# Performance work log

Hardware: AMD Instinct MI355X
Metric: run time of the kernel (lower is better)

The kernel has to match this reference:

```python
import jax, jax.numpy as jnp
import numpy as np

C, H, W = 128, 512, 512
YA, XA = 10, 10  # anchor grid; padded stats tables are (YA+2, XA+2)


def setup_inputs() -> dict:
    key = jax.random.key(0)
    k1, k2, k3 = jax.random.split(key, 3)
    x = jax.random.normal(k1, (2, C, H, W), jnp.float32)
    padded_mean_table = jax.random.normal(k2, (C, YA + 2, XA + 2), jnp.float32)
    # std table must be positive; keep away from zero
    padded_std_table = jax.random.uniform(k3, (C, YA + 2, XA + 2), jnp.float32) + 0.5
    weight = jnp.ones((1, C, 1, 1), jnp.float32)
    bias = jnp.zeros((1, C, 1, 1), jnp.float32)
    return {
        "x": x,
        "padded_mean_table": padded_mean_table,
        "padded_std_table": padded_std_table,
        "weight": weight,
        "bias": bias,
        "y_anchor": 3,
        "x_anchor": 4,
        "pre_y_anchor": 3,
        "pre_x_anchor": 5,
    }


def _axis_weights(n):
    # anchors of the 3x3 table sit at the centers of 3 tiles of size n;
    # we sample the pixels of the central tile. pos in (0.5, 1.5) in
    # anchor-index space -> bilinear between anchors (0,1) or (1,2).
    pos = (jnp.arange(n, dtype=jnp.float32) + 0.5) / n + 0.5
    i0 = jnp.floor(pos).astype(jnp.int32)  # 0 or 1
    w = pos - i0.astype(jnp.float32)
    return i0, w


def _interp3x3(table, h, w):
    # table: [C,3,3] -> [C,h,w] separable bilinear interpolation
    iy, wy = _axis_weights(h)
    ix, wx = _axis_weights(w)
    rows = table[:, iy, :] * (1.0 - wy)[None, :, None] + table[:, iy + 1, :] * wy[None, :, None]  # [C,h,3]
    out = rows[:, :, ix] * (1.0 - wx)[None, None, :] + rows[:, :, ix + 1] * wx[None, None, :]      # [C,h,w]
    return out


def reference(x, padded_mean_table, padded_std_table, weight, bias,
              y_anchor, x_anchor, pre_y_anchor, pre_x_anchor):
    real_x, pre_x = x[:1], x[1:]
    h, w = real_x.shape[2], real_x.shape[3]

    # --- pre_x branch: compute stats, scatter into padded tables, normalize ---
    pre_mean = jnp.mean(pre_x, axis=(2, 3))           # [1,C]
    pre_std = jnp.std(pre_x, axis=(2, 3), ddof=1)      # torch.std_mean default: unbiased
    pmt = padded_mean_table.at[:, pre_y_anchor + 1, pre_x_anchor + 1].set(pre_mean[0])
    pst = padded_std_table.at[:, pre_y_anchor + 1, pre_x_anchor + 1].set(pre_std[0])
    pre_out = (pre_x - pre_mean[:, :, None, None]) / pre_std[:, :, None, None] * weight + bias

    # --- real_x branch: gather 3x3 stats window, mask zeros with center, interpolate ---
    m = pmt[:, y_anchor:y_anchor + 3, x_anchor:x_anchor + 3]   # [C,3,3]
    s = pst[:, y_anchor:y_anchor + 3, x_anchor:x_anchor + 3]   # [C,3,3]
    m = jnp.where(m == 0, m[:, 1:2, 1:2], m)
    s = jnp.where(s == 0, s[:, 1:2, 1:2], s)
    m_map = _interp3x3(m, h, w)[None]          # [1,C,H,W]
    s_inv_map = _interp3x3(1.0 / s, h, w)[None]  # inverse-std interpolation
    real_out = (real_x - m_map) * s_inv_map * weight + bias

    return jnp.concatenate([real_out, pre_out], axis=0)
```

## Files before the change

### kernel.cpp

```cpp
#include <hip/hip_runtime.h>

constexpr int Cc  = 128;
constexpr int Hh  = 512;
constexpr int Ww  = 512;
constexpr int HW  = Hh * Ww;
constexpr int CHW = Cc * HW;
constexpr int NCHUNK = 16;

typedef float f32x4 __attribute__((ext_vector_type(4)));

__global__ __launch_bounds__(256) void pdin_reduce(const float* __restrict__ x,
                                                   float* __restrict__ partials) {
    const int c = blockIdx.y, chunk = blockIdx.x, tid = threadIdx.x;
    const f32x4* src = reinterpret_cast<const f32x4*>(
        x + (size_t)CHW + (size_t)c * HW + (size_t)chunk * 16384);
    float s = 0.f, q = 0.f;
#pragma unroll
    for (int i = 0; i < 16; ++i) {
        f32x4 v = src[tid + i * 256];
        s += (v.x + v.y) + (v.z + v.w);
        q += (v.x * v.x + v.y * v.y) + (v.z * v.z + v.w * v.w);
    }
#pragma unroll
    for (int off = 32; off; off >>= 1) {
        s += __shfl_down(s, off);
        q += __shfl_down(q, off);
    }
    __shared__ float ls[4], lq[4];
    const int wave = tid >> 6, lane = tid & 63;
    if (lane == 0) { ls[wave] = s; lq[wave] = q; }
    __syncthreads();
    if (tid == 0) {
        float S = (ls[0] + ls[1]) + (ls[2] + ls[3]);
        float Q = (lq[0] + lq[1]) + (lq[2] + lq[3]);
        partials[(c * NCHUNK + chunk) * 2 + 0] = S;
        partials[(c * NCHUNK + chunk) * 2 + 1] = Q;
    }
}

__global__ __launch_bounds__(256) void pdin_apply(const float* __restrict__ x,
                                                  const float* __restrict__ partials,
                                                  const float* __restrict__ mt,
                                                  const float* __restrict__ st,
                                                  const float* __restrict__ wgt,
                                                  const float* __restrict__ bia,
                                                  const int* __restrict__ ya_p,
                                                  const int* __restrict__ xa_p,
                                                  const int* __restrict__ pya_p,
                                                  const int* __restrict__ pxa_p,
                                                  float* __restrict__ out) {
    const int rblk = blockIdx.x;
    const int c    = blockIdx.y;
    const int half = blockIdx.z;

    float S = 0.f, Q = 0.f;
#pragma unroll
    for (int k = 0; k < NCHUNK; ++k) {
        S += partials[(c * NCHUNK + k) * 2 + 0];
        Q += partials[(c * NCHUNK + k) * 2 + 1];
    }
    const float Nf = (float)HW;
    const float mean = S / Nf;
    float var = (Q - S * mean) / (Nf - 1.0f);
    var = fmaxf(var, 0.0f);
    const float stdv = sqrtf(var);
    const float w = wgt[c], b = bia[c];

    const size_t cslab = (size_t)c * HW;
    const int base = rblk * 2048 + threadIdx.x;

    if (half == 0) {
        const float scale = w / stdv;
        const float shift = b - mean * scale;
        const f32x4* src = reinterpret_cast<const f32x4*>(x + (size_t)CHW + cslab);
        f32x4*       dst = reinterpret_cast<f32x4*>(out + (size_t)CHW + cslab);
        f32x4 v[8];
#pragma unroll
        for (int i = 0; i < 8; ++i) v[i] = src[base + i * 256];
#pragma unroll
        for (int i = 0; i < 8; ++i) {
            f32x4 o;
            o.x = v[i].x * scale + shift;
            o.y = v[i].y * scale + shift;
            o.z = v[i].z * scale + shift;
            o.w = v[i].w * scale + shift;
            __builtin_nontemporal_store(o, dst + base + i * 256);
        }
        return;
    }

    const int ya = ya_p[0], xa = xa_p[0];
    const int wr = pya_p[0] + 1, wc = pxa_p[0] + 1;
    const float* mtc = mt + c * 144;
    const float* stc = st + c * 144;

    const bool cw = (ya + 1 == wr) && (xa + 1 == wc);
    const float cm = cw ? mean : mtc[(ya + 1) * 12 + (xa + 1)];
    const float cs = cw ? stdv : stc[(ya + 1) * 12 + (xa + 1)];

    float G[9], R9[9];
#pragma unroll
    for (int r = 0; r < 3; ++r)
#pragma unroll
        for (int k = 0; k < 3; ++k) {
            const int Rr = ya + r, L = xa + k;
            const bool hit = (Rr == wr) && (L == wc);
            float mv = hit ? mean : mtc[Rr * 12 + L];
            if (mv == 0.0f) mv = cm;
            float sv = hit ? stdv : stc[Rr * 12 + L];
            if (sv == 0.0f) sv = cs;
            G[r * 3 + k]  = mv;
            R9[r * 3 + k] = 1.0f / sv;
        }

    const f32x4* src = reinterpret_cast<const f32x4*>(x + cslab);
    f32x4*       dst = reinterpret_cast<f32x4*>(out + cslab);
    constexpr float inv = 1.0f / 512.0f;

    f32x4 v[8];
#pragma unroll
    for (int i = 0; i < 8; ++i)
        v[i] = __builtin_nontemporal_load(src + base + i * 256);

#pragma unroll
    for (int i = 0; i < 8; ++i) {
        const int p  = base + i * 256;
        const int y  = p >> 7;
        const int xq = p & 127;
        const int iy = (y  >= 256) ? 1 : 0;
        const int ix = (xq >= 64)  ? 1 : 0;
        const float wy  = ((float)y + 0.5f) * inv + 0.5f - (float)iy;
        const float wx0 = ((float)(xq * 4) + 0.5f) * inv + 0.5f - (float)ix;

        const float a0 = iy ? G[3] : G[0], a1 = iy ? G[4] : G[1], a2 = iy ? G[5] : G[2];
        const float b0 = iy ? G[6] : G[3], b1 = iy ? G[7] : G[4], b2 = iy ? G[8] : G[5];
        const float mtL = ix ? a1 : a0, mtR = ix ? a2 : a1;
        const float mbL = ix ? b1 : b0, mbR = ix ? b2 : b1;
        const float u0 = iy ? R9[3] : R9[0], u1 = iy ? R9[4] : R9[1], u2 = iy ? R9[5] : R9[2];
        const float v0 = iy ? R9[6] : R9[3], v1 = iy ? R9[7] : R9[4], v2 = iy ? R9[8] : R9[5];
        const float stL = ix ? u1 : u0, stR = ix ? u2 : u1;
        const float sbL = ix ? v1 : v0, sbR = ix ? v2 : v1;

        const float omwy = 1.0f - wy;
        const float mrowL = mtL * omwy + mbL * wy;
        const float mrowR = mtR * omwy + mbR * wy;
        const float srowL = stL * omwy + sbL * wy;
        const float srowR = stR * omwy + sbR * wy;

        float r[4];
        const float in4[4] = { v[i].x, v[i].y, v[i].z, v[i].w };
#pragma unroll
        for (int j = 0; j < 4; ++j) {
            const float wx   = wx0 + (float)j * inv;
            const float omwx = 1.0f - wx;
            const float m_v  = mrowL * omwx + mrowR * wx;
            const float s_v  = srowL * omwx + srowR * wx;
            r[j] = (in4[j] - m_v) * s_v * w + b;
        }
        f32x4 o; o.x = r[0]; o.y = r[1]; o.z = r[2]; o.w = r[3];
        __builtin_nontemporal_store(o, dst + p);
    }
}

extern "C" void kernel_launch(void* const* d_in, const int* in_sizes, int n_in,
                              void* d_out, int out_size, void* d_ws, size_t ws_size,
                              hipStream_t stream) {
    const float* x   = (const float*)d_in[0];
    const float* mt  = (const float*)d_in[1];
    const float* st  = (const float*)d_in[2];
    const float* wgt = (const float*)d_in[3];
    const float* bia = (const float*)d_in[4];
    const int* ya  = (const int*)d_in[5];
    const int* xa  = (const int*)d_in[6];
    const int* pya = (const int*)d_in[7];
    const int* pxa = (const int*)d_in[8];
    float* out = (float*)d_out;

    float* partials = (float*)d_ws;

    pdin_reduce<<<dim3(NCHUNK, Cc), 256, 0, stream>>>(x, partials);
    pdin_apply<<<dim3(Hh / 16, Cc, 2), 256, 0, stream>>>(
        x, partials, mt, st, wgt, bia, ya, xa, pya, pxa, out);
}
```

Before: 109.3 us.

## Fuse reduce and apply into one persistent cooperative kernel with grid sync

Merges the statistics reduction and the normalization/interpolation pass into a single cooperative kernel. Persistent blocks loop over reduction chunks, meet at a grid-wide barrier, then loop over apply units. This removes the second kernel launch and the gap between the two kernels. In exchange it adds grid-sync overhead, host-side occupancy queries on every launch, and a grid capped at 2048 blocks, which may reduce memory-level parallelism.

```diff
diff --git a/kernel.cpp b/kernel.cpp
--- a/kernel.cpp
+++ b/kernel.cpp
@@ -1,4 +1,7 @@
 #include <hip/hip_runtime.h>
+#include <hip/hip_cooperative_groups.h>
+
+namespace cg = cooperative_groups;
 
 constexpr int Cc  = 128;
 constexpr int Hh  = 512;
@@ -6,159 +9,169 @@
 constexpr int HW  = Hh * Ww;
 constexpr int CHW = Cc * HW;
 constexpr int NCHUNK = 16;
+constexpr int NCHUNKS_TOTAL = Cc * NCHUNK;
+constexpr int NUNITS = 2 * Cc * 32;
 
 typedef float f32x4 __attribute__((ext_vector_type(4)));
 
-__global__ __launch_bounds__(256) void pdin_reduce(const float* __restrict__ x,
-                                                   float* __restrict__ partials) {
-    const int c = blockIdx.y, chunk = blockIdx.x, tid = threadIdx.x;
-    const f32x4* src = reinterpret_cast<const f32x4*>(
-        x + (size_t)CHW + (size_t)c * HW + (size_t)chunk * 16384);
-    float s = 0.f, q = 0.f;
-#pragma unroll
-    for (int i = 0; i < 16; ++i) {
-        f32x4 v = src[tid + i * 256];
-        s += (v.x + v.y) + (v.z + v.w);
-        q += (v.x * v.x + v.y * v.y) + (v.z * v.z + v.w * v.w);
+__global__ __launch_bounds__(256, 4) void pdin_fused(
+    const float* __restrict__ x,
+    float* __restrict__ partials,
+    const float* __restrict__ mt,
+    const float* __restrict__ st,
+    const float* __restrict__ wgt,
+    const float* __restrict__ bia,
+    const int* __restrict__ ya_p,
+    const int* __restrict__ xa_p,
+    const int* __restrict__ pya_p,
+    const int* __restrict__ pxa_p,
+    float* __restrict__ out)
+{
+    const int tid = threadIdx.x;
+    const int G   = gridDim.x;
+    __shared__ float ls[4], lq[4];
+
+    for (int cidx = blockIdx.x; cidx < NCHUNKS_TOTAL; cidx += G) {
+        const int c = cidx >> 4, chunk = cidx & 15;
+        const f32x4* src = reinterpret_cast<const f32x4*>(
+            x + (size_t)CHW + (size_t)c * HW + (size_t)chunk * 16384);
+        float s = 0.f, q = 0.f;
+#pragma unroll
+        for (int i = 0; i < 16; ++i) {
+            f32x4 v = src[tid + i * 256];
+            s += (v.x + v.y) + (v.z + v.w);
+            q += (v.x * v.x + v.y * v.y) + (v.z * v.z + v.w * v.w);
+        }
+#pragma unroll
+        for (int off = 32; off; off >>= 1) {
+            s += __shfl_down(s, off);
+            q += __shfl_down(q, off);
+        }
+        const int wave = tid >> 6, lane = tid & 63;
+        if (lane == 0) { ls[wave] = s; lq[wave] = q; }
+        __syncthreads();
+        if (tid == 0) {
+            partials[cidx * 2 + 0] = (ls[0] + ls[1]) + (ls[2] + ls[3]);
+            partials[cidx * 2 + 1] = (lq[0] + lq[1]) + (lq[2] + lq[3]);
+        }
+        __syncthreads();
     }
-#pragma unroll
-    for (int off = 32; off; off >>= 1) {
-        s += __shfl_down(s, off);
-        q += __shfl_down(q, off);
-    }
-    __shared__ float ls[4], lq[4];
-    const int wave = tid >> 6, lane = tid & 63;
-    if (lane == 0) { ls[wave] = s; lq[wave] = q; }
-    __syncthreads();
-    if (tid == 0) {
-        float S = (ls[0] + ls[1]) + (ls[2] + ls[3]);
-        float Q = (lq[0] + lq[1]) + (lq[2] + lq[3]);
-        partials[(c * NCHUNK + chunk) * 2 + 0] = S;
-        partials[(c * NCHUNK + chunk) * 2 + 1] = Q;
-    }
-}
-
-__global__ __launch_bounds__(256) void pdin_apply(const float* __restrict__ x,
-                                                  const float* __restrict__ partials,
-                                                  const float* __restrict__ mt,
-                                                  const float* __restrict__ st,
-                                                  const float* __restrict__ wgt,
-                                                  const float* __restrict__ bia,
-                                                  const int* __restrict__ ya_p,
-                                                  const int* __restrict__ xa_p,
-                                                  const int* __restrict__ pya_p,
-                                                  const int* __restrict__ pxa_p,
-                                                  float* __restrict__ out) {
-    const int rblk = blockIdx.x;
-    const int c    = blockIdx.y;
-    const int half = blockIdx.z;
-
-    float S = 0.f, Q = 0.f;
-#pragma unroll
-    for (int k = 0; k < NCHUNK; ++k) {
-        S += partials[(c * NCHUNK + k) * 2 + 0];
-        Q += partials[(c * NCHUNK + k) * 2 + 1];
-    }
-    const float Nf = (float)HW;
-    const float mean = S / Nf;
-    float var = (Q - S * mean) / (Nf - 1.0f);
-    var = fmaxf(var, 0.0f);
-    const float stdv = sqrtf(var);
-    const float w = wgt[c], b = bia[c];
-
-    const size_t cslab = (size_t)c * HW;
-    const int base = rblk * 2048 + threadIdx.x;
-
-    if (half == 0) {
-        const float scale = w / stdv;
-        const float shift = b - mean * scale;
-        const f32x4* src = reinterpret_cast<const f32x4*>(x + (size_t)CHW + cslab);
-        f32x4*       dst = reinterpret_cast<f32x4*>(out + (size_t)CHW + cslab);
+
+    cg::this_grid().sync();
+
+    for (int u = blockIdx.x; u < NUNITS; u += G) {
+        const int half = u >> 12;
+        const int rem  = u & 4095;
+        const int c    = rem >> 5;
+        const int rblk = rem & 31;
+
+        float S = 0.f, Q = 0.f;
+#pragma unroll
+        for (int k = 0; k < NCHUNK; ++k) {
+            S += partials[(c * NCHUNK + k) * 2 + 0];
+            Q += partials[(c * NCHUNK + k) * 2 + 1];
+        }
+        const float Nf = (float)HW;
+        const float mean = S / Nf;
+        float var = (Q - S * mean) / (Nf - 1.0f);
+        var = fmaxf(var, 0.0f);
+        const float stdv = sqrtf(var);
+        const float w = wgt[c], b = bia[c];
+
+        const size_t cslab = (size_t)c * HW;
+        const int base = rblk * 2048 + tid;
+
+        if (half == 0) {
+            const float scale = w / stdv;
+            const float shift = b - mean * scale;
+            const f32x4* src = reinterpret_cast<const f32x4*>(x + (size_t)CHW + cslab);
+            f32x4*       dst = reinterpret_cast<f32x4*>(out + (size_t)CHW + cslab);
+            f32x4 v[8];
+#pragma unroll
+            for (int i = 0; i < 8; ++i) v[i] = src[base + i * 256];
+#pragma unroll
+            for (int i = 0; i < 8; ++i) {
+                f32x4 o;
+                o.x = v[i].x * scale + shift;
+                o.y = v[i].y * scale + shift;
+                o.z = v[i].z * scale + shift;
+                o.w = v[i].w * scale + shift;
+                __builtin_nontemporal_store(o, dst + base + i * 256);
+            }
+            continue;
+        }
+
+        const int ya = ya_p[0], xa = xa_p[0];
+        const int wr = pya_p[0] + 1, wc = pxa_p[0] + 1;
+        const float* mtc = mt + c * 144;
+        const float* stc = st + c * 144;
+
+        const bool cwh = (ya + 1 == wr) && (xa + 1 == wc);
+        const float cm = cwh ? mean : mtc[(ya + 1) * 12 + (xa + 1)];
+        const float cs = cwh ? stdv : stc[(ya + 1) * 12 + (xa + 1)];
+
+        float Gm[9], R9[9];
+#pragma unroll
+        for (int r = 0; r < 3; ++r)
+#pragma unroll
+            for (int k = 0; k < 3; ++k) {
+                const int Rr = ya + r, L = xa + k;
+                const bool hit = (Rr == wr) && (L == wc);
+                float mv = hit ? mean : mtc[Rr * 12 + L];
+                if (mv == 0.0f) mv = cm;
+                float sv = hit ? stdv : stc[Rr * 12 + L];
+                if (sv == 0.0f) sv = cs;
+                Gm[r * 3 + k] = mv;
+                R9[r * 3 + k] = 1.0f / sv;
+            }
+
+        const f32x4* src = reinterpret_cast<const f32x4*>(x + cslab);
+        f32x4*       dst = reinterpret_cast<f32x4*>(out + cslab);
+        constexpr float inv = 1.0f / 512.0f;
+
         f32x4 v[8];
 #pragma unroll
-        for (int i = 0; i < 8; ++i) v[i] = src[base + i * 256];
+        for (int i = 0; i < 8; ++i)
+            v[i] = __builtin_nontemporal_load(src + base + i * 256);
+
 #pragma unroll
         for (int i = 0; i < 8; ++i) {
-            f32x4 o;
-            o.x = v[i].x * scale + shift;
-            o.y = v[i].y * scale + shift;
-            o.z = v[i].z * scale + shift;
-            o.w = v[i].w * scale + shift;
-            __builtin_nontemporal_store(o, dst + base + i * 256);
-        }
-        return;
-    }
-
-    const int ya = ya_p[0], xa = xa_p[0];
-    const int wr = pya_p[0] + 1, wc = pxa_p[0] + 1;
-    const float* mtc = mt + c * 144;
-    const float* stc = st + c * 144;
-
-    const bool cw = (ya + 1 == wr) && (xa + 1 == wc);
-    const float cm = cw ? mean : mtc[(ya + 1) * 12 + (xa + 1)];
-    const float cs = cw ? stdv : stc[(ya + 1) * 12 + (xa + 1)];
-
-    float G[9], R9[9];
-#pragma unroll
-    for (int r = 0; r < 3; ++r)
-#pragma unroll
-        for (int k = 0; k < 3; ++k) {
-            const int Rr = ya + r, L = xa + k;
-            const bool hit = (Rr == wr) && (L == wc);
-            float mv = hit ? mean : mtc[Rr * 12 + L];
-            if (mv == 0.0f) mv = cm;
-            float sv = hit ? stdv : stc[Rr * 12 + L];
-            if (sv == 0.0f) sv = cs;
-            G[r * 3 + k]  = mv;
-            R9[r * 3 + k] = 1.0f / sv;
-        }
-
-    const f32x4* src = reinterpret_cast<const f32x4*>(x + cslab);
-    f32x4*       dst = reinterpret_cast<f32x4*>(out + cslab);
-    constexpr float inv = 1.0f / 512.0f;
-
-    f32x4 v[8];
-#pragma unroll
-    for (int i = 0; i < 8; ++i)
-        v[i] = __builtin_nontemporal_load(src + base + i * 256);
-
-#pragma unroll
-    for (int i = 0; i < 8; ++i) {
-        const int p  = base + i * 256;
-        const int y  = p >> 7;
-        const int xq = p & 127;
-        const int iy = (y  >= 256) ? 1 : 0;
-        const int ix = (xq >= 64)  ? 1 : 0;
-        const float wy  = ((float)y + 0.5f) * inv + 0.5f - (float)iy;
-        const float wx0 = ((float)(xq * 4) + 0.5f) * inv + 0.5f - (float)ix;
-
-        const float a0 = iy ? G[3] : G[0], a1 = iy ? G[4] : G[1], a2 = iy ? G[5] : G[2];
-        const float b0 = iy ? G[6] : G[3], b1 = iy ? G[7] : G[4], b2 = iy ? G[8] : G[5];
-        const float mtL = ix ? a1 : a0, mtR = ix ? a2 : a1;
-        const float mbL = ix ? b1 : b0, mbR = ix ? b2 : b1;
-        const float u0 = iy ? R9[3] : R9[0], u1 = iy ? R9[4] : R9[1], u2 = iy ? R9[5] : R9[2];
-        const float v0 = iy ? R9[6] : R9[3], v1 = iy ? R9[7] : R9[4], v2 = iy ? R9[8] : R9[5];
-        const float stL = ix ? u1 : u0, stR = ix ? u2 : u1;
-        const float sbL = ix ? v1 : v0, sbR = ix ? v2 : v1;
-
-        const float omwy = 1.0f - wy;
-        const float mrowL = mtL * omwy + mbL * wy;
-        const float mrowR = mtR * omwy + mbR * wy;
-        const float srowL = stL * omwy + sbL * wy;
-        const float srowR = stR * omwy + sbR * wy;
-
-        float r[4];
-        const float in4[4] = { v[i].x, v[i].y, v[i].z, v[i].w };
-#pragma unroll
-        for (int j = 0; j < 4; ++j) {
-            const float wx   = wx0 + (float)j * inv;
-            const float omwx = 1.0f - wx;
-            const float m_v  = mrowL * omwx + mrowR * wx;
-            const float s_v  = srowL * omwx + srowR * wx;
-            r[j] = (in4[j] - m_v) * s_v * w + b;
-        }
-        f32x4 o; o.x = r[0]; o.y = r[1]; o.z = r[2]; o.w = r[3];
-        __builtin_nontemporal_store(o, dst + p);
+            const int p  = base + i * 256;
+            const int y  = p >> 7;
+            const int xq = p & 127;
+            const int iy = (y  >= 256) ? 1 : 0;
+            const int ix = (xq >= 64)  ? 1 : 0;
+            const float wy  = ((float)y + 0.5f) * inv + 0.5f - (float)iy;
+            const float wx0 = ((float)(xq * 4) + 0.5f) * inv + 0.5f - (float)ix;
+
+            const float a0 = iy ? Gm[3] : Gm[0], a1 = iy ? Gm[4] : Gm[1], a2 = iy ? Gm[5] : Gm[2];
+            const float b0 = iy ? Gm[6] : Gm[3], b1 = iy ? Gm[7] : Gm[4], b2 = iy ? Gm[8] : Gm[5];
+            const float mtL = ix ? a1 : a0, mtR = ix ? a2 : a1;
+            const float mbL = ix ? b1 : b0, mbR = ix ? b2 : b1;
+            const float u0 = iy ? R9[3] : R9[0], u1 = iy ? R9[4] : R9[1], u2 = iy ? R9[5] : R9[2];
+            const float v0 = iy ? R9[6] : R9[3], v1 = iy ? R9[7] : R9[4], v2 = iy ? R9[8] : R9[5];
+            const float stL = ix ? u1 : u0, stR = ix ? u2 : u1;
+            const float sbL = ix ? v1 : v0, sbR = ix ? v2 : v1;
+
+            const float omwy = 1.0f - wy;
+            const float mrowL = mtL * omwy + mbL * wy;
+            const float mrowR = mtR * omwy + mbR * wy;
+            const float srowL = stL * omwy + sbL * wy;
+            const float srowR = stR * omwy + sbR * wy;
+
+            float r[4];
+            const float in4[4] = { v[i].x, v[i].y, v[i].z, v[i].w };
+#pragma unroll
+            for (int j = 0; j < 4; ++j) {
+                const float wx   = wx0 + (float)j * inv;
+                const float omwx = 1.0f - wx;
+                const float m_v  = mrowL * omwx + mrowR * wx;
+                const float s_v  = srowL * omwx + srowR * wx;
+                r[j] = (in4[j] - m_v) * s_v * w + b;
+            }
+            f32x4 o; o.x = r[0]; o.y = r[1]; o.z = r[2]; o.w = r[3];
+            __builtin_nontemporal_store(o, dst + p);
+        }
     }
 }
 
@@ -175,10 +188,21 @@
     const int* pya = (const int*)d_in[7];
     const int* pxa = (const int*)d_in[8];
     float* out = (float*)d_out;
-
     float* partials = (float*)d_ws;
 
-    pdin_reduce<<<dim3(NCHUNK, Cc), 256, 0, stream>>>(x, partials);
-    pdin_apply<<<dim3(Hh / 16, Cc, 2), 256, 0, stream>>>(
-        x, partials, mt, st, wgt, bia, ya, xa, pya, pxa, out);
+    int dev = 0;
+    hipGetDevice(&dev);
+    int nCU = 256;
+    hipDeviceGetAttribute(&nCU, hipDeviceAttributeMultiprocessorCount, dev);
+    int perCU = 0;
+    hipOccupancyMaxActiveBlocksPerMultiprocessor(&perCU, pdin_fused, 256, 0);
+    if (perCU < 1) perCU = 1;
+    int G = nCU * perCU;
+    if (G > NCHUNKS_TOTAL) G = NCHUNKS_TOTAL;
+
+    void* args[] = { (void*)&x, (void*)&partials, (void*)&mt, (void*)&st,
+                     (void*)&wgt, (void*)&bia, (void*)&ya, (void*)&xa,
+                     (void*)&pya, (void*)&pxa, (void*)&out };
+    hipLaunchCooperativeKernel((void*)pdin_fused, dim3(G), dim3(256),
+                               args, 0, stream);
 }
```

After: 190.4 us. 1.74x slower.
